# Performance work log

Hardware: AMD Instinct MI355X
Metric: run time of the kernel (lower is better)

The kernel has to match this reference:

```python
import jax, jax.numpy as jnp
import numpy as np

N, E, F, K = 20000, 320000, 256, 3


def setup_inputs() -> dict:
    key = jax.random.key(0)
    ks = jax.random.split(key, 10)
    x = jax.random.normal(ks[0], (N, F), jnp.float32)
    edge_index = jax.random.randint(ks[1], (2, E), 0, N)
    edge_weight = jax.random.uniform(ks[2], (E,), jnp.float32)
    h = jax.random.normal(ks[3], (N, F), jnp.float32)
    c = jax.random.normal(ks[4], (N, F), jnp.float32)
    s = 1.0 / np.sqrt(F)
    W = jax.random.normal(ks[5], (4, F, F), jnp.float32) * s        # x->gate (i,f,c,o)
    theta = jax.random.normal(ks[6], (4, K, F, F), jnp.float32) * s  # Cheb weights per gate
    b_conv = jnp.zeros((4, F), jnp.float32)                          # ChebConv biases
    b = jnp.zeros((4, F), jnp.float32)                               # gate biases
    w_c = jax.random.normal(ks[7], (3, F), jnp.float32) * s          # peephole (i,f,o)
    W_cls = jax.random.normal(ks[8], (F, 1), jnp.float32) * s
    b_cls = jnp.zeros((1,), jnp.float32)
    return dict(x=x, edge_index=edge_index, edge_weight=edge_weight, h=h, c=c,
                W=W, theta=theta, b_conv=b_conv, b=b, w_c=w_c, W_cls=W_cls, b_cls=b_cls)


def _cheb(h, src, dst, wnorm, theta_g, b_g):
    # ChebConv with sym normalization, lambda_max=2: L_hat = -D^{-1/2} A D^{-1/2}
    n = h.shape[0]

    def prop(v):  # (L_hat v)[dst] = sum_e wnorm[e] * v[src[e]]
        return jax.ops.segment_sum(wnorm[:, None] * v[src], dst, num_segments=n)

    Tx0 = h
    out = Tx0 @ theta_g[0]
    Tx1 = prop(h)
    out = out + Tx1 @ theta_g[1]
    for k in range(2, theta_g.shape[0]):
        Tx2 = 2.0 * prop(Tx1) - Tx0
        out = out + Tx2 @ theta_g[k]
        Tx0, Tx1 = Tx1, Tx2
    return out + b_g


def _gclstm(x, src, dst, wnorm, h, c, W, theta, b_conv, b, w_c):
    conv = lambda g: _cheb(h, src, dst, wnorm, theta[g], b_conv[g])
    i = jax.nn.sigmoid(x @ W[0] + conv(0) + w_c[0] * c + b[0])
    f = jax.nn.sigmoid(x @ W[1] + conv(1) + w_c[1] * c + b[1])
    t = jnp.tanh(x @ W[2] + conv(2) + b[2])
    c_new = f * c + i * t
    o = jax.nn.sigmoid(x @ W[3] + conv(3) + w_c[2] * c_new + b[3])
    h_new = o * jnp.tanh(c_new)
    return h_new, c_new


def reference(x, edge_index, edge_weight, h, c, W, theta, b_conv, b, w_c, W_cls, b_cls):
    src, dst = edge_index[0], edge_index[1]
    deg = jax.ops.segment_sum(edge_weight, src, num_segments=x.shape[0])
    dis = jnp.where(deg > 0, jax.lax.rsqrt(jnp.maximum(deg, 1e-12)), 0.0)
    wnorm = -dis[src] * edge_weight * dis[dst]
    h0, c0 = _gclstm(x, src, dst, wnorm, h, c, W, theta, b_conv, b, w_c)
    out = jax.nn.relu(h0) @ W_cls + b_cls  # [N, 1]
    return out, h0, c0
```

## Files before the change

### kernel.cpp

```cpp
#include <hip/hip_runtime.h>
#include <stdint.h>

#define FDIM 256
#define KDIM 1024

typedef __attribute__((ext_vector_type(8))) short short8;
typedef __attribute__((ext_vector_type(4))) float floatx4;

#define GLOBAL_AS __attribute__((address_space(1)))
#define LDS_AS    __attribute__((address_space(3)))

static __device__ __forceinline__ unsigned short f2bf(float f) {
    unsigned int u = __float_as_uint(f);
    unsigned int r = (u + 0x7FFFu + ((u >> 16) & 1u)) >> 16;
    return (unsigned short)r;
}
static __device__ __forceinline__ float bf2f(unsigned short s) {
    return __uint_as_float(((unsigned int)s) << 16);
}
static __device__ __forceinline__ float sig(float x) {
    return 1.f / (1.f + __expf(-x));
}


__global__ void k_degcnt(const int* __restrict__ src, const int* __restrict__ dst,
                         const float* __restrict__ ew, float* deg, int* cnt, int e) {
    int i = blockIdx.x * blockDim.x + threadIdx.x;
    if (i < e) {
        atomicAdd(&deg[src[i]], ew[i]);
        atomicAdd(&cnt[dst[i]], 1);
    }
}

__launch_bounds__(1024)
__global__ void k_scan1(const int* __restrict__ cnt, int* __restrict__ offs,
                        int* __restrict__ part, int n) {
    __shared__ int wsum[16];
    int b = blockIdx.x;
    int i = b * 1024 + (int)threadIdx.x;
    int lane = threadIdx.x & 63;
    int wid = threadIdx.x >> 6;
    int x = (i < n) ? cnt[i] : 0;
#pragma unroll
    for (int s = 1; s < 64; s <<= 1) {
        int t = __shfl_up(x, s);
        if (lane >= s) x += t;
    }
    if (lane == 63) wsum[wid] = x;
    __syncthreads();
    if (wid == 0) {
        int y = (lane < 16) ? wsum[lane] : 0;
#pragma unroll
        for (int s = 1; s < 16; s <<= 1) {
            int t = __shfl_up(y, s);
            if (lane >= s) y += t;
        }
        if (lane < 16) wsum[lane] = y;
    }
    __syncthreads();
    int wbase = (wid > 0) ? wsum[wid - 1] : 0;
    if (i < n) offs[i + 1] = wbase + x;
    if (threadIdx.x == 1023) part[b] = wsum[15];
}

__launch_bounds__(1024)
__global__ void k_scan2(int* __restrict__ offs, const int* __restrict__ part, int n) {
    __shared__ int sprefix;
    int b = blockIdx.x;
    if (threadIdx.x < 64) {
        int p = ((int)threadIdx.x < b) ? part[threadIdx.x] : 0;
#pragma unroll
        for (int s = 32; s; s >>= 1) p += __shfl_down(p, s);
        if (threadIdx.x == 0) sprefix = p;
    }
    __syncthreads();
    int i = b * 1024 + (int)threadIdx.x;
    if (i < n) offs[i + 1] += sprefix;
    if (b == 0 && threadIdx.x == 0) offs[0] = 0;
}

__global__ void k_scatter(const int* __restrict__ src, const int* __restrict__ dst,
                          const float* __restrict__ ew, const float* __restrict__ deg,
                          const int* __restrict__ offs, int* cur,
                          int2* __restrict__ csr, int e) {
    int i = blockIdx.x * blockDim.x + threadIdx.x;
    if (i < e) {
        int s = src[i], d = dst[i];
        float ds_ = deg[s], dd = deg[d];
        float rs = ds_ > 0.f ? rsqrtf(fmaxf(ds_, 1e-12f)) : 0.f;
        float rd = dd > 0.f ? rsqrtf(fmaxf(dd, 1e-12f)) : 0.f;
        float wn = -rs * ew[i] * rd;
        int pos = offs[d] + atomicAdd(&cur[d], 1);
        csr[pos] = make_int2(s, __float_as_int(wn));
    }
}


__global__ void k_packA(const float* __restrict__ x, const float* __restrict__ h,
                        unsigned short* __restrict__ A, int n) {
    int t = blockIdx.x * blockDim.x + threadIdx.x;
    int node = t >> 6, q = t & 63;
    if (node >= n) return;
    floatx4 xv = *(const floatx4*)(x + (size_t)node * FDIM + q * 4);
    floatx4 hv = *(const floatx4*)(h + (size_t)node * FDIM + q * 4);
    ushort4 ox, oh;
    ox.x = f2bf(xv[0]); ox.y = f2bf(xv[1]); ox.z = f2bf(xv[2]); ox.w = f2bf(xv[3]);
    oh.x = f2bf(hv[0]); oh.y = f2bf(hv[1]); oh.z = f2bf(hv[2]); oh.w = f2bf(hv[3]);
    *(ushort4*)(A + (size_t)node * KDIM + q * 4) = ox;
    *(ushort4*)(A + (size_t)node * KDIM + FDIM + q * 4) = oh;
}

__global__ void k_packBt(const float* __restrict__ W, const float* __restrict__ theta,
                         unsigned short* __restrict__ Bt) {
    int t = blockIdx.x * blockDim.x + threadIdx.x;
    int p = t >> 10, r = t & 1023;
    int group = p >> 6, gate = (p >> 4) & 3;
    int feat = (group << 4) | (p & 15);
    int kb = r >> 8, rr = r & 255;
    float v;
    if (kb == 0) v = W[((size_t)(gate * FDIM + rr)) * FDIM + feat];
    else         v = theta[((size_t)((gate * 3 + (kb - 1)) * FDIM + rr)) * FDIM + feat];
    Bt[t] = f2bf(v);
}


__launch_bounds__(256)
__global__ void k_prop1(unsigned short* __restrict__ A, const int* __restrict__ offs,
                        const int2* __restrict__ csr, int n) {
    int wid = (blockIdx.x * blockDim.x + threadIdx.x) >> 6;
    int lane = threadIdx.x & 63;
    if (wid >= n) return;
    int half = lane >> 5, l = lane & 31;
    int beg = offs[wid], end = offs[wid + 1];
    float a[8] = {0.f, 0.f, 0.f, 0.f, 0.f, 0.f, 0.f, 0.f};
    int j = beg + half;
    for (; j + 6 < end; j += 8) {
        int2 e0 = csr[j], e1 = csr[j + 2], e2 = csr[j + 4], e3 = csr[j + 6];
        short8 v0 = *(const short8*)(A + (size_t)e0.x * KDIM + FDIM + l * 8);
        short8 v1 = *(const short8*)(A + (size_t)e1.x * KDIM + FDIM + l * 8);
        short8 v2 = *(const short8*)(A + (size_t)e2.x * KDIM + FDIM + l * 8);
        short8 v3 = *(const short8*)(A + (size_t)e3.x * KDIM + FDIM + l * 8);
        float w0 = __int_as_float(e0.y), w1 = __int_as_float(e1.y);
        float w2 = __int_as_float(e2.y), w3 = __int_as_float(e3.y);
#pragma unroll
        for (int k = 0; k < 8; ++k)
            a[k] += w0 * bf2f((unsigned short)v0[k]) + w1 * bf2f((unsigned short)v1[k])
                  + w2 * bf2f((unsigned short)v2[k]) + w3 * bf2f((unsigned short)v3[k]);
    }
    for (; j < end; j += 2) {
        int2 e0 = csr[j];
        float w0 = __int_as_float(e0.y);
        short8 v0 = *(const short8*)(A + (size_t)e0.x * KDIM + FDIM + l * 8);
#pragma unroll
        for (int k = 0; k < 8; ++k) a[k] += w0 * bf2f((unsigned short)v0[k]);
    }
#pragma unroll
    for (int k = 0; k < 8; ++k) a[k] += __shfl_xor(a[k], 32);
    if (half == 0) {
        short8 o;
#pragma unroll
        for (int k = 0; k < 8; ++k) o[k] = (short)f2bf(a[k]);
        *(short8*)(A + (size_t)wid * KDIM + 2 * FDIM + l * 8) = o;
    }
}

__launch_bounds__(256)
__global__ void k_prop2(unsigned short* __restrict__ A, const float* __restrict__ h,
                        const int* __restrict__ offs, const int2* __restrict__ csr, int n) {
    int wid = (blockIdx.x * blockDim.x + threadIdx.x) >> 6;
    int lane = threadIdx.x & 63;
    if (wid >= n) return;
    int half = lane >> 5, l = lane & 31;
    int beg = offs[wid], end = offs[wid + 1];
    float a[8] = {0.f, 0.f, 0.f, 0.f, 0.f, 0.f, 0.f, 0.f};
    int j = beg + half;
    for (; j + 6 < end; j += 8) {
        int2 e0 = csr[j], e1 = csr[j + 2], e2 = csr[j + 4], e3 = csr[j + 6];
        short8 v0 = *(const short8*)(A + (size_t)e0.x * KDIM + 2 * FDIM + l * 8);
        short8 v1 = *(const short8*)(A + (size_t)e1.x * KDIM + 2 * FDIM + l * 8);
        short8 v2 = *(const short8*)(A + (size_t)e2.x * KDIM + 2 * FDIM + l * 8);
        short8 v3 = *(const short8*)(A + (size_t)e3.x * KDIM + 2 * FDIM + l * 8);
        float w0 = __int_as_float(e0.y), w1 = __int_as_float(e1.y);
        float w2 = __int_as_float(e2.y), w3 = __int_as_float(e3.y);
#pragma unroll
        for (int k = 0; k < 8; ++k)
            a[k] += w0 * bf2f((unsigned short)v0[k]) + w1 * bf2f((unsigned short)v1[k])
                  + w2 * bf2f((unsigned short)v2[k]) + w3 * bf2f((unsigned short)v3[k]);
    }
    for (; j < end; j += 2) {
        int2 e0 = csr[j];
        float w0 = __int_as_float(e0.y);
        short8 v0 = *(const short8*)(A + (size_t)e0.x * KDIM + 2 * FDIM + l * 8);
#pragma unroll
        for (int k = 0; k < 8; ++k) a[k] += w0 * bf2f((unsigned short)v0[k]);
    }
#pragma unroll
    for (int k = 0; k < 8; ++k) a[k] += __shfl_xor(a[k], 32);
    if (half == 0) {
        floatx4 hv0 = *(const floatx4*)(h + (size_t)wid * FDIM + l * 8);
        floatx4 hv1 = *(const floatx4*)(h + (size_t)wid * FDIM + l * 8 + 4);
        short8 o;
#pragma unroll
        for (int k = 0; k < 4; ++k) o[k] = (short)f2bf(2.f * a[k] - hv0[k]);
#pragma unroll
        for (int k = 0; k < 4; ++k) o[4 + k] = (short)f2bf(2.f * a[4 + k] - hv1[k]);
        *(short8*)(A + (size_t)wid * KDIM + 3 * FDIM + l * 8) = o;
    }
}


__launch_bounds__(256, 2)
__global__ void k_gemm(const unsigned short* __restrict__ A, const unsigned short* __restrict__ Bt,
                       const float* __restrict__ c, const float* __restrict__ b_conv,
                       const float* __restrict__ b, const float* __restrict__ w_c,
                       const float* __restrict__ Wcls,
                       float* __restrict__ out_h, float* __restrict__ out_c,
                       float* __restrict__ cls_part, int M, int mtiles) {
    __shared__ unsigned short sA[2][128 * 64];
    __shared__ unsigned short sB[2][128 * 64];
    int tid = threadIdx.x;
    int lane = tid & 63;
    int w = tid >> 6;
    int nb = mtiles * 8;
    int bid = blockIdx.x;
    int wg = (bid & 7) * (nb >> 3) + (bid >> 3);
    int mt = wg >> 3;
    int nt = wg & 7;
    int brow = mt * 128, bcol = nt * 128;
    int wr = (w >> 1) * 64, wc = (w & 1) * 64;
    int l15 = lane & 15, l4 = lane >> 4;

    auto STAGE = [&](int kt, int bufi) {
        int k0 = kt * 64;
#pragma unroll
        for (int p = 0; p < 4; ++p) {
            int cch = tid + p * 256;
            int row = cch >> 3, cslot = cch & 7;
            int csrc = cslot ^ (row & 7);
            int grow = brow + row; if (grow >= M) grow = M - 1;
            const unsigned short* g = A + (size_t)grow * KDIM + k0 + csrc * 8;
            __builtin_amdgcn_global_load_lds((const GLOBAL_AS void*)g,
                                             (LDS_AS void*)(sA[bufi] + cch * 8), 16, 0, 0);
        }
#pragma unroll
        for (int p = 0; p < 4; ++p) {
            int cch = tid + p * 256;
            int row = cch >> 3, cslot = cch & 7;
            int csrc = cslot ^ (row & 7);
            const unsigned short* g = Bt + (size_t)(bcol + row) * KDIM + k0 + csrc * 8;
            __builtin_amdgcn_global_load_lds((const GLOBAL_AS void*)g,
                                             (LDS_AS void*)(sB[bufi] + cch * 8), 16, 0, 0);
        }
    };

    floatx4 acc[4][4];
#pragma unroll
    for (int m = 0; m < 4; ++m)
#pragma unroll
        for (int g = 0; g < 4; ++g)
            acc[m][g] = (floatx4){0.f, 0.f, 0.f, 0.f};

    STAGE(0, 0);

    for (int kt = 0; kt < 16; ++kt) {
        int cur = kt & 1;
        if (kt < 15) {
            STAGE(kt + 1, cur ^ 1);
            asm volatile("s_waitcnt vmcnt(8)" ::: "memory");
        } else {
            asm volatile("s_waitcnt vmcnt(0)" ::: "memory");
        }
        __builtin_amdgcn_s_barrier();
        __builtin_amdgcn_sched_barrier(0);

#pragma unroll
        for (int ks = 0; ks < 2; ++ks) {
            short8 af[4], bfr[4];
#pragma unroll
            for (int m = 0; m < 4; ++m) {
                int ra = wr + m * 16 + l15;
                af[m] = *(const short8*)(sA[cur] + ra * 64 + ((ks * 4 + l4) ^ (ra & 7)) * 8);
            }
#pragma unroll
            for (int g = 0; g < 4; ++g) {
                int rb = wc + g * 16 + l15;
                bfr[g] = *(const short8*)(sB[cur] + rb * 64 + ((ks * 4 + l4) ^ (rb & 7)) * 8);
            }
#pragma unroll
            for (int m = 0; m < 4; ++m)
#pragma unroll
                for (int g = 0; g < 4; ++g)
                    acc[m][g] = __builtin_amdgcn_mfma_f32_16x16x32_bf16(af[m], bfr[g], acc[m][g], 0, 0, 0);
        }
        asm volatile("s_waitcnt lgkmcnt(0)" ::: "memory");
        __builtin_amdgcn_sched_barrier(0);
        __builtin_amdgcn_s_barrier();
    }

    int group = (bcol + wc) >> 6;
    int feat = (group << 4) | l15;
    float bc0 = b_conv[feat], bc1 = b_conv[FDIM + feat];
    float bc2 = b_conv[2 * FDIM + feat], bc3 = b_conv[3 * FDIM + feat];
    float bb0 = b[feat], bb1 = b[FDIM + feat];
    float bb2 = b[2 * FDIM + feat], bb3 = b[3 * FDIM + feat];
    float wci = w_c[feat], wcf = w_c[FDIM + feat], wco = w_c[2 * FDIM + feat];
    float wcl = Wcls[feat];

#pragma unroll
    for (int m = 0; m < 4; ++m) {
#pragma unroll
        for (int j = 0; j < 4; ++j) {
            int node = brow + wr + m * 16 + l4 * 4 + j;
            bool ok = node < M;
            int nidx = ok ? node : (M - 1);
            float cv = c[(size_t)nidx * FDIM + feat];
            float iv = sig(acc[m][0][j] + bc0 + wci * cv + bb0);
            float fv = sig(acc[m][1][j] + bc1 + wcf * cv + bb1);
            float tv = tanhf(acc[m][2][j] + bc2 + bb2);
            float cn = fv * cv + iv * tv;
            float ov = sig(acc[m][3][j] + bc3 + wco * cn + bb3);
            float hn = ov * tanhf(cn);
            if (ok) {
                out_h[(size_t)node * FDIM + feat] = hn;
                out_c[(size_t)node * FDIM + feat] = cn;
            }
            float pcls = fmaxf(hn, 0.f) * wcl;
#pragma unroll
            for (int s = 1; s < 16; s <<= 1) pcls += __shfl_xor(pcls, s);
            if (ok && l15 == 0) cls_part[(size_t)node * 16 + group] = pcls;
        }
    }
}

__global__ void k_cls(const float* __restrict__ cls_part, const float* __restrict__ bcls,
                      float* __restrict__ out_cls, int n) {
    int i = blockIdx.x * blockDim.x + threadIdx.x;
    if (i >= n) return;
    const floatx4* p = (const floatx4*)(cls_part + (size_t)i * 16);
    floatx4 v0 = p[0], v1 = p[1], v2 = p[2], v3 = p[3];
    float s = v0[0] + v0[1] + v0[2] + v0[3] + v1[0] + v1[1] + v1[2] + v1[3]
            + v2[0] + v2[1] + v2[2] + v2[3] + v3[0] + v3[1] + v3[2] + v3[3];
    out_cls[i] = s + bcls[0];
}


extern "C" void kernel_launch(void* const* d_in, const int* in_sizes, int n_in,
                              void* d_out, int out_size, void* d_ws, size_t ws_size,
                              hipStream_t stream) {
    const float* x      = (const float*)d_in[0];
    const int*   eidx   = (const int*)d_in[1];
    const float* ew     = (const float*)d_in[2];
    const float* h      = (const float*)d_in[3];
    const float* c      = (const float*)d_in[4];
    const float* W      = (const float*)d_in[5];
    const float* theta  = (const float*)d_in[6];
    const float* b_conv = (const float*)d_in[7];
    const float* b      = (const float*)d_in[8];
    const float* w_c    = (const float*)d_in[9];
    const float* Wcls   = (const float*)d_in[10];
    const float* bcls   = (const float*)d_in[11];

    const int N = in_sizes[0] / FDIM;
    const int E = in_sizes[2];
    const int* src = eidx;
    const int* dst = eidx + E;

    char* ws = (char*)d_ws;
    size_t off = 0;
    auto alloc = [&](size_t bytes) -> void* {
        void* p = ws + off;
        off += (bytes + 255) & ~(size_t)255;
        return p;
    };
    unsigned short* A   = (unsigned short*)alloc((size_t)N * KDIM * 2);
    unsigned short* Bt  = (unsigned short*)alloc((size_t)KDIM * KDIM * 2);
    float* cls_part     = (float*)alloc((size_t)N * 16 * 4);
    float* deg          = (float*)alloc((size_t)N * 4);
    int*   cnt          = (int*)alloc((size_t)N * 4);
    int*   cur          = (int*)alloc((size_t)N * 4);
    int*   offs         = (int*)alloc((size_t)(N + 1) * 4);
    int*   part         = (int*)alloc(64 * 4);
    int2*  csr          = (int2*)alloc((size_t)E * 8);
    (void)ws_size; (void)n_in; (void)out_size;

    float* out_cls = (float*)d_out;
    float* out_h   = out_cls + N;
    float* out_c   = out_h + (size_t)N * FDIM;

    size_t zbytes = (size_t)((char*)(cur + N) - (char*)deg);
    hipMemsetAsync(deg, 0, zbytes, stream);

    int nsb = (N + 1023) / 1024;
    k_degcnt<<<(E + 255) / 256, 256, 0, stream>>>(src, dst, ew, deg, cnt, E);
    k_scan1<<<nsb, 1024, 0, stream>>>(cnt, offs, part, N);
    k_scan2<<<nsb, 1024, 0, stream>>>(offs, part, N);
    k_scatter<<<(E + 255) / 256, 256, 0, stream>>>(src, dst, ew, deg, offs, cur, csr, E);
    k_packA<<<(N * 64 + 255) / 256, 256, 0, stream>>>(x, h, A, N);
    k_packBt<<<(KDIM * KDIM + 255) / 256, 256, 0, stream>>>(W, theta, Bt);
    k_prop1<<<(N * 64 + 255) / 256, 256, 0, stream>>>(A, offs, csr, N);
    k_prop2<<<(N * 64 + 255) / 256, 256, 0, stream>>>(A, h, offs, csr, N);
    int mtiles = (N + 127) / 128;
    k_gemm<<<mtiles * 8, 256, 0, stream>>>(A, Bt, c, b_conv, b, w_c, Wcls,
                                           out_h, out_c, cls_part, N, mtiles);
    k_cls<<<(N + 255) / 256, 256, 0, stream>>>(cls_part, bcls, out_cls, N);
}
```

Baseline: 211.7 us.

## Pre-swizzle B into MFMA fragment order and load it directly from global

The weight matrix is packed so each wave's MFMA B fragments sit contiguously in fragment order. The GEMM then reads B straight from global or L2 into registers instead of staging it through LDS. This halves LDS use, which allows launch bounds of 3 blocks per CU, and replaces the manual waitcnt and barrier pipeline with a single __syncthreads per k-step. The cost is that global B loads now sit in the critical path of each iteration, and their latency may be less well hidden than with the old double-buffered LDS copy.

```diff
diff --git a/kernel.cpp b/kernel.cpp
--- a/kernel.cpp
+++ b/kernel.cpp
@@ -113,7 +113,13 @@
 __global__ void k_packBt(const float* __restrict__ W, const float* __restrict__ theta,
                          unsigned short* __restrict__ Bt) {
     int t = blockIdx.x * blockDim.x + threadIdx.x;
-    int p = t >> 10, r = t & 1023;
+    int e = t & 7;
+    int lane = (t >> 3) & 63;
+    int ks = (t >> 9) & 1;
+    int kt = (t >> 10) & 15;
+    int pg = t >> 14;
+    int p = pg * 16 + (lane & 15);
+    int r = kt * 64 + ks * 32 + (lane >> 4) * 8 + e;
     int group = p >> 6, gate = (p >> 4) & 3;
     int feat = (group << 4) | (p & 15);
     int kb = r >> 8, rr = r & 255;
@@ -209,15 +215,14 @@
 }
 
 
-__launch_bounds__(256, 2)
-__global__ void k_gemm(const unsigned short* __restrict__ A, const unsigned short* __restrict__ Bt,
+__launch_bounds__(256, 3)
+__global__ void k_gemm(const unsigned short* __restrict__ A, const unsigned short* __restrict__ Bf,
                        const float* __restrict__ c, const float* __restrict__ b_conv,
                        const float* __restrict__ b, const float* __restrict__ w_c,
                        const float* __restrict__ Wcls,
                        float* __restrict__ out_h, float* __restrict__ out_c,
                        float* __restrict__ cls_part, int M, int mtiles) {
     __shared__ unsigned short sA[2][128 * 64];
-    __shared__ unsigned short sB[2][128 * 64];
     int tid = threadIdx.x;
     int lane = tid & 63;
     int w = tid >> 6;
@@ -230,7 +235,10 @@
     int wr = (w >> 1) * 64, wc = (w & 1) * 64;
     int l15 = lane & 15, l4 = lane >> 4;
 
-    auto STAGE = [&](int kt, int bufi) {
+    int pgbase = nt * 8 + (w & 1) * 4;
+    const unsigned short* Bwave = Bf + (size_t)pgbase * 32 * 64 * 8;
+
+    auto STAGE_A = [&](int kt, int bufi) {
         int k0 = kt * 64;
 #pragma unroll
         for (int p = 0; p < 4; ++p) {
@@ -242,15 +250,6 @@
             __builtin_amdgcn_global_load_lds((const GLOBAL_AS void*)g,
                                              (LDS_AS void*)(sA[bufi] + cch * 8), 16, 0, 0);
         }
-#pragma unroll
-        for (int p = 0; p < 4; ++p) {
-            int cch = tid + p * 256;
-            int row = cch >> 3, cslot = cch & 7;
-            int csrc = cslot ^ (row & 7);
-            const unsigned short* g = Bt + (size_t)(bcol + row) * KDIM + k0 + csrc * 8;
-            __builtin_amdgcn_global_load_lds((const GLOBAL_AS void*)g,
-                                             (LDS_AS void*)(sB[bufi] + cch * 8), 16, 0, 0);
-        }
     };
 
     floatx4 acc[4][4];
@@ -260,41 +259,35 @@
         for (int g = 0; g < 4; ++g)
             acc[m][g] = (floatx4){0.f, 0.f, 0.f, 0.f};
 
-    STAGE(0, 0);
+    STAGE_A(0, 0);
 
     for (int kt = 0; kt < 16; ++kt) {
         int cur = kt & 1;
-        if (kt < 15) {
-            STAGE(kt + 1, cur ^ 1);
-            asm volatile("s_waitcnt vmcnt(8)" ::: "memory");
-        } else {
-            asm volatile("s_waitcnt vmcnt(0)" ::: "memory");
-        }
-        __builtin_amdgcn_s_barrier();
-        __builtin_amdgcn_sched_barrier(0);
+        __syncthreads();
+        if (kt < 15) STAGE_A(kt + 1, cur ^ 1);
+
+        short8 bfr[2][4];
+#pragma unroll
+        for (int ks = 0; ks < 2; ++ks)
+#pragma unroll
+            for (int g = 0; g < 4; ++g)
+                bfr[ks][g] = *(const short8*)(Bwave +
+                    (size_t)(((g * 32 + kt * 2 + ks) * 64) + lane) * 8);
 
 #pragma unroll
         for (int ks = 0; ks < 2; ++ks) {
-            short8 af[4], bfr[4];
+            short8 af[4];
 #pragma unroll
             for (int m = 0; m < 4; ++m) {
                 int ra = wr + m * 16 + l15;
                 af[m] = *(const short8*)(sA[cur] + ra * 64 + ((ks * 4 + l4) ^ (ra & 7)) * 8);
             }
 #pragma unroll
-            for (int g = 0; g < 4; ++g) {
-                int rb = wc + g * 16 + l15;
-                bfr[g] = *(const short8*)(sB[cur] + rb * 64 + ((ks * 4 + l4) ^ (rb & 7)) * 8);
-            }
-#pragma unroll
             for (int m = 0; m < 4; ++m)
 #pragma unroll
                 for (int g = 0; g < 4; ++g)
-                    acc[m][g] = __builtin_amdgcn_mfma_f32_16x16x32_bf16(af[m], bfr[g], acc[m][g], 0, 0, 0);
+                    acc[m][g] = __builtin_amdgcn_mfma_f32_16x16x32_bf16(af[m], bfr[ks][g], acc[m][g], 0, 0, 0);
         }
-        asm volatile("s_waitcnt lgkmcnt(0)" ::: "memory");
-        __builtin_amdgcn_sched_barrier(0);
-        __builtin_amdgcn_s_barrier();
     }
 
     int group = (bcol + wc) >> 6;
```

Result: faster. 200.0 us (-5.5%).
